# Kernel tuning notes

Measured on AMD Instinct MI355X. Metric: run time of the kernel, lower is better.

## Reference

```python
import jax, jax.numpy as jnp
import numpy as np

N, C, H, L = 10000, 256, 8, 3
D = C // H  # per-head dim
E = 320000


def setup_inputs() -> dict:
    key = jax.random.key(0)
    ks = jax.random.split(key, 12)
    x = jax.random.normal(ks[0], (N, C), dtype=jnp.float32)
    edge_index = jax.random.randint(ks[1], (2, E), 0, N, dtype=jnp.int64)
    s = 0.02
    Wq = jax.random.normal(ks[2], (L, C, C), dtype=jnp.float32) * s
    Wk = jax.random.normal(ks[3], (L, C, C), dtype=jnp.float32) * s
    Wv = jax.random.normal(ks[4], (L, C, C), dtype=jnp.float32) * s
    Ws = jax.random.normal(ks[5], (L, C, C), dtype=jnp.float32) * s
    bq = jax.random.normal(ks[6], (L, C), dtype=jnp.float32) * s
    bk = jax.random.normal(ks[7], (L, C), dtype=jnp.float32) * s
    bv = jax.random.normal(ks[8], (L, C), dtype=jnp.float32) * s
    bs = jax.random.normal(ks[9], (L, C), dtype=jnp.float32) * s
    return {"x": x, "Wq": Wq, "bq": bq, "Wk": Wk, "bk": bk,
            "Wv": Wv, "bv": bv, "Ws": Ws, "bs": bs, "edge_index": edge_index}


def _transformer_conv(x, Wq, bq, Wk, bk, Wv, bv, Ws, bs, src, dst):
    # projections: [N, C] -> [N, H, D]
    q = (x @ Wq + bq).reshape(N, H, D)
    k = (x @ Wk + bk).reshape(N, H, D)
    v = (x @ Wv + bv).reshape(N, H, D)
    # per-edge attention scores: query at target, key/value at source
    score = jnp.einsum('ehd,ehd->eh', q[dst], k[src]) / jnp.sqrt(jnp.float32(D))  # [E, H]
    # scatter softmax over incoming edges per target node
    m = jax.ops.segment_max(score, dst, num_segments=N)            # [N, H]
    a = jnp.exp(score - m[dst])                                    # [E, H]
    denom = jax.ops.segment_sum(a, dst, num_segments=N)           # [N, H]
    alpha = a / (denom[dst] + 1e-16)                               # [E, H]
    # weighted aggregation of values
    msg = alpha[:, :, None] * v[src]                               # [E, H, D]
    out = jax.ops.segment_sum(msg, dst, num_segments=N).reshape(N, C)
    # root/skip connection
    return out + x @ Ws + bs


def reference(x, Wq, bq, Wk, bk, Wv, bv, Ws, bs, edge_index):
    src, dst = edge_index[0], edge_index[1]
    for l in range(L):
        x = _transformer_conv(x, Wq[l], bq[l], Wk[l], bk[l],
                              Wv[l], bv[l], Ws[l], bs[l], src, dst)
    return x
```

## Files before the change

kernel.cpp:

```cpp
#include <hip/hip_runtime.h>
#include <hip/hip_bf16.h>

#define N_NODES 10000
#define C_DIM   256
#define H_HEADS 8
#define D_HEAD  32
#define E_EDGES 320000
#define L_LAYERS 3
#define GN      1024

typedef __attribute__((ext_vector_type(8))) short bf16x8;
typedef __attribute__((ext_vector_type(4))) float f32x4;

__device__ __forceinline__ unsigned short f2b(float f) {
  __hip_bfloat16 h = __float2bfloat16(f);
  return *(unsigned short*)&h;
}

__device__ __forceinline__ float kv_lo(unsigned int w) {
  union { unsigned int u; float f; } c; c.u = w << 16; return c.f;
}
__device__ __forceinline__ float kv_hi(unsigned int w) {
  union { unsigned int u; float f; } c; c.u = w & 0xffff0000u; return c.f;
}

__device__ __forceinline__ float red8(float p) {
  p += __shfl_xor(p, 1);
  p += __shfl_xor(p, 2);
  p += __shfl_xor(p, 4);
  return p;
}

__device__ __forceinline__ float dot4(float4 q, uint4 w) {
  return fmaf(q.x, kv_lo(w.x),
         fmaf(q.y, kv_lo(w.y),
         fmaf(q.z, kv_lo(w.z), q.w * kv_lo(w.w))));
}

__device__ __forceinline__ void gload16(const void* g, void* l) {
  __builtin_amdgcn_global_load_lds(
      (const __attribute__((address_space(1))) unsigned int*)g,
      (__attribute__((address_space(3))) unsigned int*)l, 16, 0, 0);
}

__device__ __forceinline__ int colmap(int mat, int c) {
  if (mat == 0) return c;
  if (mat == 3) return 768 + c;
  return 256 + ((c >> 6) << 7) + ((mat - 1) << 6) + (c & 63);
}

__global__ void hist_kernel(const int* __restrict__ dst, int* __restrict__ deg) {
  int e = blockIdx.x * blockDim.x + threadIdx.x;
  if (e < E_EDGES) atomicAdd(&deg[dst[e]], 1);
}

__global__ __launch_bounds__(1024) void scan_kernel(const int* __restrict__ deg,
                                                    int* __restrict__ row_ptr) {
  __shared__ int part[1024];
  int t = threadIdx.x;
  const int CHUNK = (N_NODES + 1023) / 1024;
  int base = t * CHUNK;
  int s = 0;
  for (int i = 0; i < CHUNK; ++i) {
    int idx = base + i;
    if (idx < N_NODES) s += deg[idx];
  }
  part[t] = s;
  __syncthreads();
  for (int off = 1; off < 1024; off <<= 1) {
    int v = (t >= off) ? part[t - off] : 0;
    __syncthreads();
    part[t] += v;
    __syncthreads();
  }
  int run = (t == 0) ? 0 : part[t - 1];
  for (int i = 0; i < CHUNK; ++i) {
    int idx = base + i;
    if (idx <= N_NODES) {
      row_ptr[idx] = run;
      if (idx < N_NODES) run += deg[idx];
    }
  }
}

__global__ void scatter_kernel(const int* __restrict__ src, const int* __restrict__ dst,
                               const int* __restrict__ row_ptr, int* __restrict__ fill,
                               int* __restrict__ srcs) {
  int e = blockIdx.x * blockDim.x + threadIdx.x;
  if (e < E_EDGES) {
    int d = dst[e];
    int pos = atomicAdd(&fill[d], 1);
    srcs[row_ptr[d] + pos] = src[e];
  }
}

__global__ __launch_bounds__(256) void conv_all_kernel(
    const float* __restrict__ x, __hip_bfloat16* __restrict__ xb,
    const float* __restrict__ Wq, const float* __restrict__ Wk,
    const float* __restrict__ Wv, const float* __restrict__ Ws,
    __hip_bfloat16* __restrict__ Wt,
    const float* __restrict__ bq, const float* __restrict__ bk,
    const float* __restrict__ bv, const float* __restrict__ bs,
    float* __restrict__ biasf) {
  __shared__ float tt[32][33];
  int b = blockIdx.x, t = threadIdx.x;
  if (b < 2500) {
    int i = b * 256 + t;
    float4 f = *(const float4*)&x[(size_t)i * 4];
    union { unsigned short u[4]; uint2 w; } o;
    o.u[0] = f2b(f.x); o.u[1] = f2b(f.y); o.u[2] = f2b(f.z); o.u[3] = f2b(f.w);
    *(uint2*)&xb[(size_t)i * 4] = o.w;
  } else if (b < 3268) {
    int zz = b - 2500;
    int z = zz >> 6, tile = zz & 63;
    int l = z >> 2, mat = z & 3;
    const float* W = (mat == 0 ? Wq : mat == 1 ? Wk : mat == 2 ? Wv : Ws)
                     + (size_t)l * C_DIM * C_DIM;
    int k0 = (tile >> 3) * 32, c0 = (tile & 7) * 32;
    int tx = t & 31, ty = t >> 5;
    for (int i = 0; i < 32; i += 8)
      tt[ty + i][tx] = W[(k0 + ty + i) * C_DIM + c0 + tx];
    __syncthreads();
    for (int i = 0; i < 32; i += 8) {
      int ncol = colmap(mat, c0 + ty + i);
      Wt[(size_t)l * GN * C_DIM + (size_t)ncol * C_DIM + k0 + tx] =
          __float2bfloat16(tt[tx][ty + i]);
    }
  } else {
    int i = (b - 3268) * 256 + t;
    if (i < L_LAYERS * GN) {
      int l = i >> 10, n = i & 1023;
      int mat = n >> 8, c = n & 255;
      const float* bb = (mat == 0 ? bq : mat == 1 ? bk : mat == 2 ? bv : bs);
      biasf[l * GN + colmap(mat, c)] = bb[l * C_DIM + c];
    }
  }
}

__global__ __launch_bounds__(256) void gemm_kernel(
    const __hip_bfloat16* __restrict__ xb,
    const __hip_bfloat16* __restrict__ Wt,
    const float* __restrict__ biasf,
    float* __restrict__ q2,
    unsigned short* __restrict__ kvu,
    float* __restrict__ skip) {
  __shared__ __align__(16) unsigned short SH[16384];
  __hip_bfloat16* As = (__hip_bfloat16*)SH;
  __hip_bfloat16* Bs = (__hip_bfloat16*)(SH + 8192);
  int tid = threadIdx.x;
  int wid = tid >> 6, lane = tid & 63;
  int row0 = blockIdx.x * 128;
  int col0 = blockIdx.y * 128;
  int wr = wid >> 1, wc = wid & 1;
  int lr = lane & 15, lq = lane >> 4;
  int swz = (lr & 7) * 8;

  f32x4 acc[4][4] = {};

  for (int k0 = 0; k0 < C_DIM; k0 += 64) {
#pragma unroll
    for (int j = 0; j < 4; ++j) {
      int c = j * 256 + wid * 64 + lane;
      int arow = c >> 3;
      int kc = 8 * ((c & 7) ^ ((c >> 3) & 7));
      int grow = row0 + arow;
      if (grow > N_NODES - 1) grow = N_NODES - 1;
      gload16(xb + (size_t)grow * C_DIM + k0 + kc, As + (size_t)(j * 256 + wid * 64) * 8);
    }
#pragma unroll
    for (int j = 0; j < 4; ++j) {
      int c = j * 256 + wid * 64 + lane;
      int brow = c >> 3;
      int kc = 8 * ((c & 7) ^ ((c >> 3) & 7));
      gload16(Wt + (size_t)(col0 + brow) * C_DIM + k0 + kc,
              Bs + (size_t)(j * 256 + wid * 64) * 8);
    }
    __syncthreads();

#pragma unroll
    for (int ks = 0; ks < 2; ++ks) {
      bf16x8 fa[4], fb[4];
#pragma unroll
      for (int m = 0; m < 4; ++m)
        fa[m] = *(const bf16x8*)&As[(wr * 64 + m * 16 + lr) * 64 + ((ks * 32 + lq * 8) ^ swz)];
#pragma unroll
      for (int n = 0; n < 4; ++n)
        fb[n] = *(const bf16x8*)&Bs[(wc * 64 + n * 16 + lr) * 64 + ((ks * 32 + lq * 8) ^ swz)];
#pragma unroll
      for (int m = 0; m < 4; ++m)
#pragma unroll
        for (int n = 0; n < 4; ++n)
          acc[m][n] = __builtin_amdgcn_mfma_f32_16x16x32_bf16(fa[m], fb[n], acc[m][n], 0, 0, 0);
    }
    __syncthreads();
  }

  float bias_n[4];
#pragma unroll
  for (int n = 0; n < 4; ++n) bias_n[n] = biasf[col0 + wc * 64 + n * 16 + lr];

  if (col0 >= 256 && col0 < 768) {
    int half = wc;
#pragma unroll
    for (int m = 0; m < 4; ++m) {
#pragma unroll
      for (int n = 0; n < 4; ++n) {
        int chs = n * 16 + lr;
#pragma unroll
        for (int r = 0; r < 4; ++r) {
          int row = wr * 64 + m * 16 + lq * 4 + r;
          SH[row * 128 + chs * 2 + half] = f2b(acc[m][n][r] + bias_n[n]);
        }
      }
    }
    __syncthreads();
    int bl = (col0 - 256) >> 7;
    int sl = bl >> 1;
    int h64 = (bl & 1) * 64;
    unsigned int* kvd = (unsigned int*)kvu;
    int t16 = tid & 15, rbase = tid >> 4;
#pragma unroll
    for (int it = 0; it < 8; ++it) {
      int row = it * 16 + rbase;
      int grow = row0 + row;
      if (grow < N_NODES) {
        uint4 vv = *(const uint4*)&SH[row * 128 + t16 * 8];
        *(uint4*)&kvd[((size_t)sl * N_NODES + grow) * 128 + h64 + t16 * 4] = vv;
      }
    }
  } else {
#pragma unroll
    for (int m = 0; m < 4; ++m) {
#pragma unroll
      for (int n = 0; n < 4; ++n) {
        int colG = col0 + wc * 64 + n * 16 + lr;
#pragma unroll
        for (int r = 0; r < 4; ++r) {
          int grow = row0 + wr * 64 + m * 16 + lq * 4 + r;
          if (grow < N_NODES) {
            float val = acc[m][n][r] + bias_n[n];
            if (col0 < 256) {
              q2[((size_t)(colG >> 7) * N_NODES + grow) * 128 + (colG & 127)] = val;
            } else {
              skip[(size_t)grow * C_DIM + (colG - 768)] = val;
            }
          }
        }
      }
    }
  }
}

__global__ __launch_bounds__(256) void agg_kernel(
    const float* __restrict__ q2,
    const unsigned int* __restrict__ kv2,
    const int* __restrict__ row_ptr, const int* __restrict__ srcs,
    float* __restrict__ out, __hip_bfloat16* __restrict__ xb_next) {
  int b = blockIdx.x;
  int slice = b & 1;
  int wid = threadIdx.x >> 6, lane = threadIdx.x & 63;
  int n = (b >> 1) * 4 + wid;
  int slot = lane >> 5;
  int l4 = (lane & 31) * 4;
  const size_t SB = (size_t)slice * N_NODES * 128;
  const float scl = 0.25503526f;

  float4 qv = *(const float4*)&q2[SB + (size_t)n * 128 + l4];
  qv.x *= scl; qv.y *= scl; qv.z *= scl; qv.w *= scl;
  const unsigned int* kvs = kv2 + SB;

  int beg = row_ptr[n], end = row_ptr[n + 1];
  float l = 0.f;
  float4 a = make_float4(0.f, 0.f, 0.f, 0.f);

  int i = beg;
  int sa1 = 0, sb1 = 0;
  uint4 wa = make_uint4(0, 0, 0, 0), wb = make_uint4(0, 0, 0, 0);
  if (i + 4 <= end) {
    int sa0 = srcs[i + slot], sb0 = srcs[i + 2 + slot];
    wa = *(const uint4*)&kvs[(size_t)sa0 * 128 + l4];
    wb = *(const uint4*)&kvs[(size_t)sb0 * 128 + l4];
    if (i + 8 <= end) { sa1 = srcs[i + 4 + slot]; sb1 = srcs[i + 6 + slot]; }
  }
  while (i + 4 <= end) {
    uint4 na = make_uint4(0, 0, 0, 0), nb = make_uint4(0, 0, 0, 0);
    if (i + 8 <= end) {
      na = *(const uint4*)&kvs[(size_t)sa1 * 128 + l4];
      nb = *(const uint4*)&kvs[(size_t)sb1 * 128 + l4];
      if (i + 12 <= end) {
        sa1 = srcs[i + 8 + slot]; sb1 = srcs[i + 10 + slot];
      }
    }
    float pa = red8(dot4(qv, wa));
    float pb = red8(dot4(qv, wb));
    float ea = exp2f(pa), eb = exp2f(pb);
    l += ea + eb;
    a.x = fmaf(ea, kv_hi(wa.x), fmaf(eb, kv_hi(wb.x), a.x));
    a.y = fmaf(ea, kv_hi(wa.y), fmaf(eb, kv_hi(wb.y), a.y));
    a.z = fmaf(ea, kv_hi(wa.z), fmaf(eb, kv_hi(wb.z), a.z));
    a.w = fmaf(ea, kv_hi(wa.w), fmaf(eb, kv_hi(wb.w), a.w));
    wa = na; wb = nb;
    i += 4;
  }
  for (; i < end; i += 2) {
    int j = i + slot;
    bool valid = j < end;
    int s = srcs[valid ? j : beg];
    uint4 w = *(const uint4*)&kvs[(size_t)s * 128 + l4];
    float p = red8(dot4(qv, w));
    float e = valid ? exp2f(p) : 0.f;
    l += e;
    a.x = fmaf(e, kv_hi(w.x), a.x);
    a.y = fmaf(e, kv_hi(w.y), a.y);
    a.z = fmaf(e, kv_hi(w.z), a.z);
    a.w = fmaf(e, kv_hi(w.w), a.w);
  }

  l   += __shfl_xor(l, 32);
  a.x += __shfl_xor(a.x, 32);
  a.y += __shfl_xor(a.y, 32);
  a.z += __shfl_xor(a.z, 32);
  a.w += __shfl_xor(a.w, 32);

  if (lane < 32) {
    float inv = 1.f / (l + 1e-16f);
    size_t idx = (size_t)n * C_DIM + slice * 128 + l4;
    float4 o = *(const float4*)&out[idx];
    o.x += a.x * inv; o.y += a.y * inv; o.z += a.z * inv; o.w += a.w * inv;
    *(float4*)&out[idx] = o;
    union { unsigned short us[4]; uint2 w; } ob;
    ob.us[0] = f2b(o.x); ob.us[1] = f2b(o.y); ob.us[2] = f2b(o.z); ob.us[3] = f2b(o.w);
    *(uint2*)&xb_next[idx] = ob.w;
  }
}

extern "C" void kernel_launch(void* const* d_in, const int* in_sizes, int n_in,
                              void* d_out, int out_size, void* d_ws, size_t ws_size,
                              hipStream_t stream) {
  const float* x0 = (const float*)d_in[0];
  const float* Wq = (const float*)d_in[1];
  const float* bq = (const float*)d_in[2];
  const float* Wk = (const float*)d_in[3];
  const float* bk = (const float*)d_in[4];
  const float* Wv = (const float*)d_in[5];
  const float* bv = (const float*)d_in[6];
  const float* Ws = (const float*)d_in[7];
  const float* bs = (const float*)d_in[8];
  const int* ei  = (const int*)d_in[9];
  const int* src = ei;
  const int* dst = ei + E_EDGES;
  float* out = (float*)d_out;

  const size_t NC = (size_t)N_NODES * C_DIM;
  __hip_bfloat16* xb = (__hip_bfloat16*)d_ws;
  unsigned int* kvbuf = (unsigned int*)(xb + NC);
  __hip_bfloat16* Wt = (__hip_bfloat16*)(kvbuf + NC);
  float* qbuf  = (float*)(Wt + (size_t)L_LAYERS * GN * C_DIM);
  float* skipA = qbuf + NC;
  float* biasf = skipA + NC;
  int* row_ptr = (int*)(biasf + L_LAYERS * GN);
  int* deg  = row_ptr + (N_NODES + 1);
  int* fill = deg + N_NODES;
  int* srcs = fill + N_NODES;

  (void)hipMemsetAsync(deg, 0, 2 * N_NODES * sizeof(int), stream);
  hist_kernel<<<(E_EDGES + 255) / 256, 256, 0, stream>>>(dst, deg);
  scan_kernel<<<1, 1024, 0, stream>>>(deg, row_ptr);
  scatter_kernel<<<(E_EDGES + 255) / 256, 256, 0, stream>>>(src, dst, row_ptr, fill, srcs);

  conv_all_kernel<<<3281, 256, 0, stream>>>(x0, xb, Wq, Wk, Wv, Ws, Wt,
                                            bq, bk, bv, bs, biasf);

  for (int l = 0; l < L_LAYERS; ++l) {
    float* skip = (l == L_LAYERS - 1) ? out : skipA;
    gemm_kernel<<<dim3((N_NODES + 127) / 128, GN / 128), 256, 0, stream>>>(
        xb, Wt + (size_t)l * GN * C_DIM, biasf + l * GN, qbuf,
        (unsigned short*)kvbuf, skip);
    agg_kernel<<<dim3(2 * (N_NODES / 4)), 256, 0, stream>>>(
        qbuf, kvbuf, row_ptr, srcs, skip, xb);
  }
}
```

Measured before the change: 201.5 us.

## Split fused attention aggregation into separate score and aggregation kernels with K/V split

Splits the interleaved K/V bf16 buffer into separate K and V arrays, and replaces the single fused score+softmax+aggregate kernel with two passes. The first computes exp scores per edge and head, storing them and per-node denominators. The second gathers V rows weighted by the stored scores. Each gather now reads contiguous 16-byte rows of only K or only V, with 16 lanes per edge and 4 edges in flight. The cost is an extra kernel launch, a round-trip of per-edge scores through global memory, and re-reading the CSR indices.

```diff
diff --git a/kernel.cpp b/kernel.cpp
--- a/kernel.cpp
+++ b/kernel.cpp
@@ -22,19 +22,6 @@
 }
 __device__ __forceinline__ float kv_hi(unsigned int w) {
   union { unsigned int u; float f; } c; c.u = w & 0xffff0000u; return c.f;
-}
-
-__device__ __forceinline__ float red8(float p) {
-  p += __shfl_xor(p, 1);
-  p += __shfl_xor(p, 2);
-  p += __shfl_xor(p, 4);
-  return p;
-}
-
-__device__ __forceinline__ float dot4(float4 q, uint4 w) {
-  return fmaf(q.x, kv_lo(w.x),
-         fmaf(q.y, kv_lo(w.y),
-         fmaf(q.z, kv_lo(w.z), q.w * kv_lo(w.w))));
 }
 
 __device__ __forceinline__ void gload16(const void* g, void* l) {
@@ -142,7 +129,8 @@
     const __hip_bfloat16* __restrict__ Wt,
     const float* __restrict__ biasf,
     float* __restrict__ q2,
-    unsigned short* __restrict__ kvu,
+    unsigned short* __restrict__ k2,
+    unsigned short* __restrict__ v2,
     float* __restrict__ skip) {
   __shared__ __align__(16) unsigned short SH[16384];
   __hip_bfloat16* As = (__hip_bfloat16*)SH;
@@ -209,7 +197,7 @@
 #pragma unroll
         for (int r = 0; r < 4; ++r) {
           int row = wr * 64 + m * 16 + lq * 4 + r;
-          SH[row * 128 + chs * 2 + half] = f2b(acc[m][n][r] + bias_n[n]);
+          SH[row * 128 + half * 64 + chs] = f2b(acc[m][n][r] + bias_n[n]);
         }
       }
     }
@@ -217,7 +205,6 @@
     int bl = (col0 - 256) >> 7;
     int sl = bl >> 1;
     int h64 = (bl & 1) * 64;
-    unsigned int* kvd = (unsigned int*)kvu;
     int t16 = tid & 15, rbase = tid >> 4;
 #pragma unroll
     for (int it = 0; it < 8; ++it) {
@@ -225,7 +212,10 @@
       int grow = row0 + row;
       if (grow < N_NODES) {
         uint4 vv = *(const uint4*)&SH[row * 128 + t16 * 8];
-        *(uint4*)&kvd[((size_t)sl * N_NODES + grow) * 128 + h64 + t16 * 4] = vv;
+        size_t base = ((size_t)sl * N_NODES + grow) * 128 + h64;
+        unsigned short* dp = (t16 < 8) ? (k2 + base + t16 * 8)
+                                       : (v2 + base + (t16 - 8) * 8);
+        *(uint4*)dp = vv;
       }
     }
   } else {
@@ -251,86 +241,140 @@
   }
 }
 
-__global__ __launch_bounds__(256) void agg_kernel(
+__global__ __launch_bounds__(256) void score_kernel(
     const float* __restrict__ q2,
-    const unsigned int* __restrict__ kv2,
+    const unsigned short* __restrict__ k2,
+    const int* __restrict__ row_ptr, const int* __restrict__ srcs,
+    float* __restrict__ esc,
+    float* __restrict__ dnm) {
+  int b = blockIdx.x;
+  int slice = b & 1;
+  int wid = threadIdx.x >> 6, lane = threadIdx.x & 63;
+  int n = (b >> 1) * 4 + wid;
+  int slot = lane >> 4;
+  int le = lane & 15;
+  int h = le >> 2;
+  const float scl = 0.25503526f;
+  const unsigned short* ks = k2 + (size_t)slice * N_NODES * 128;
+  float* escS = esc + (size_t)slice * E_EDGES * 4;
+
+  const float* qrow = &q2[((size_t)slice * N_NODES + n) * 128 + le * 8];
+  float4 qa = *(const float4*)qrow;
+  float4 qb = *(const float4*)(qrow + 4);
+  qa.x *= scl; qa.y *= scl; qa.z *= scl; qa.w *= scl;
+  qb.x *= scl; qb.y *= scl; qb.z *= scl; qb.w *= scl;
+
+  int beg = row_ptr[n], end = row_ptr[n + 1];
+  float l = 0.f;
+
+  if (beg < end) {
+    int j0 = beg + slot;
+    int sc = srcs[j0 < end ? j0 : beg];
+    uint4 w = *(const uint4*)&ks[(size_t)sc * 128 + le * 8];
+    int j1 = beg + 4 + slot;
+    int sn = srcs[j1 < end ? j1 : beg];
+    for (int i = beg; i < end; i += 4) {
+      uint4 wn = w;
+      bool more = (i + 4) < end;
+      if (more) {
+        wn = *(const uint4*)&ks[(size_t)sn * 128 + le * 8];
+        int j2 = i + 8 + slot;
+        sn = srcs[j2 < end ? j2 : beg];
+      }
+      float p = fmaf(qa.x, kv_lo(w.x), fmaf(qa.y, kv_hi(w.x),
+                fmaf(qa.z, kv_lo(w.y), fmaf(qa.w, kv_hi(w.y),
+                fmaf(qb.x, kv_lo(w.z), fmaf(qb.y, kv_hi(w.z),
+                fmaf(qb.z, kv_lo(w.w), qb.w * kv_hi(w.w))))))));
+      p += __shfl_xor(p, 1);
+      p += __shfl_xor(p, 2);
+      bool valid = (i + slot) < end;
+      float e = valid ? exp2f(p) : 0.f;
+      l += e;
+      if (valid && (lane & 3) == 0)
+        escS[(size_t)(i + slot) * 4 + h] = e;
+      w = wn;
+    }
+  }
+  l += __shfl_xor(l, 16);
+  l += __shfl_xor(l, 32);
+  if (lane < 16 && (lane & 3) == 0)
+    dnm[((size_t)slice * N_NODES + n) * 4 + h] = l;
+}
+
+__global__ __launch_bounds__(256) void aggr_kernel(
+    const unsigned short* __restrict__ v2,
+    const float* __restrict__ esc,
+    const float* __restrict__ dnm,
     const int* __restrict__ row_ptr, const int* __restrict__ srcs,
     float* __restrict__ out, __hip_bfloat16* __restrict__ xb_next) {
   int b = blockIdx.x;
   int slice = b & 1;
   int wid = threadIdx.x >> 6, lane = threadIdx.x & 63;
   int n = (b >> 1) * 4 + wid;
-  int slot = lane >> 5;
-  int l4 = (lane & 31) * 4;
-  const size_t SB = (size_t)slice * N_NODES * 128;
-  const float scl = 0.25503526f;
-
-  float4 qv = *(const float4*)&q2[SB + (size_t)n * 128 + l4];
-  qv.x *= scl; qv.y *= scl; qv.z *= scl; qv.w *= scl;
-  const unsigned int* kvs = kv2 + SB;
+  int slot = lane >> 4;
+  int le = lane & 15;
+  int h = le >> 2;
+  const unsigned short* vs = v2 + (size_t)slice * N_NODES * 128;
+  const float* escS = esc + (size_t)slice * E_EDGES * 4;
+
+  float inv = 1.f / (dnm[((size_t)slice * N_NODES + n) * 4 + h] + 1e-16f);
 
   int beg = row_ptr[n], end = row_ptr[n + 1];
-  float l = 0.f;
-  float4 a = make_float4(0.f, 0.f, 0.f, 0.f);
-
-  int i = beg;
-  int sa1 = 0, sb1 = 0;
-  uint4 wa = make_uint4(0, 0, 0, 0), wb = make_uint4(0, 0, 0, 0);
-  if (i + 4 <= end) {
-    int sa0 = srcs[i + slot], sb0 = srcs[i + 2 + slot];
-    wa = *(const uint4*)&kvs[(size_t)sa0 * 128 + l4];
-    wb = *(const uint4*)&kvs[(size_t)sb0 * 128 + l4];
-    if (i + 8 <= end) { sa1 = srcs[i + 4 + slot]; sb1 = srcs[i + 6 + slot]; }
-  }
-  while (i + 4 <= end) {
-    uint4 na = make_uint4(0, 0, 0, 0), nb = make_uint4(0, 0, 0, 0);
-    if (i + 8 <= end) {
-      na = *(const uint4*)&kvs[(size_t)sa1 * 128 + l4];
-      nb = *(const uint4*)&kvs[(size_t)sb1 * 128 + l4];
-      if (i + 12 <= end) {
-        sa1 = srcs[i + 8 + slot]; sb1 = srcs[i + 10 + slot];
+  float a0 = 0.f, a1 = 0.f, a2 = 0.f, a3 = 0.f;
+  float a4 = 0.f, a5 = 0.f, a6 = 0.f, a7 = 0.f;
+
+  if (beg < end) {
+    int j0 = beg + slot;
+    int jc = j0 < end ? j0 : beg;
+    int sc = srcs[jc];
+    uint4 w = *(const uint4*)&vs[(size_t)sc * 128 + le * 8];
+    float ec = escS[(size_t)jc * 4 + h];
+    int j1 = beg + 4 + slot;
+    int jn = j1 < end ? j1 : beg;
+    int sn = srcs[jn];
+    for (int i = beg; i < end; i += 4) {
+      uint4 wn = w; float en = 0.f;
+      bool more = (i + 4) < end;
+      if (more) {
+        wn = *(const uint4*)&vs[(size_t)sn * 128 + le * 8];
+        en = escS[(size_t)jn * 4 + h];
+        int j2 = i + 8 + slot;
+        jn = j2 < end ? j2 : beg;
+        sn = srcs[jn];
       }
-    }
-    float pa = red8(dot4(qv, wa));
-    float pb = red8(dot4(qv, wb));
-    float ea = exp2f(pa), eb = exp2f(pb);
-    l += ea + eb;
-    a.x = fmaf(ea, kv_hi(wa.x), fmaf(eb, kv_hi(wb.x), a.x));
-    a.y = fmaf(ea, kv_hi(wa.y), fmaf(eb, kv_hi(wb.y), a.y));
-    a.z = fmaf(ea, kv_hi(wa.z), fmaf(eb, kv_hi(wb.z), a.z));
-    a.w = fmaf(ea, kv_hi(wa.w), fmaf(eb, kv_hi(wb.w), a.w));
-    wa = na; wb = nb;
-    i += 4;
-  }
-  for (; i < end; i += 2) {
-    int j = i + slot;
-    bool valid = j < end;
-    int s = srcs[valid ? j : beg];
-    uint4 w = *(const uint4*)&kvs[(size_t)s * 128 + l4];
-    float p = red8(dot4(qv, w));
-    float e = valid ? exp2f(p) : 0.f;
-    l += e;
-    a.x = fmaf(e, kv_hi(w.x), a.x);
-    a.y = fmaf(e, kv_hi(w.y), a.y);
-    a.z = fmaf(e, kv_hi(w.z), a.z);
-    a.w = fmaf(e, kv_hi(w.w), a.w);
-  }
-
-  l   += __shfl_xor(l, 32);
-  a.x += __shfl_xor(a.x, 32);
-  a.y += __shfl_xor(a.y, 32);
-  a.z += __shfl_xor(a.z, 32);
-  a.w += __shfl_xor(a.w, 32);
-
-  if (lane < 32) {
-    float inv = 1.f / (l + 1e-16f);
-    size_t idx = (size_t)n * C_DIM + slice * 128 + l4;
-    float4 o = *(const float4*)&out[idx];
-    o.x += a.x * inv; o.y += a.y * inv; o.z += a.z * inv; o.w += a.w * inv;
-    *(float4*)&out[idx] = o;
-    union { unsigned short us[4]; uint2 w; } ob;
-    ob.us[0] = f2b(o.x); ob.us[1] = f2b(o.y); ob.us[2] = f2b(o.z); ob.us[3] = f2b(o.w);
-    *(uint2*)&xb_next[idx] = ob.w;
+      float e = ((i + slot) < end) ? ec : 0.f;
+      a0 = fmaf(e, kv_lo(w.x), a0);
+      a1 = fmaf(e, kv_hi(w.x), a1);
+      a2 = fmaf(e, kv_lo(w.y), a2);
+      a3 = fmaf(e, kv_hi(w.y), a3);
+      a4 = fmaf(e, kv_lo(w.z), a4);
+      a5 = fmaf(e, kv_hi(w.z), a5);
+      a6 = fmaf(e, kv_lo(w.w), a6);
+      a7 = fmaf(e, kv_hi(w.w), a7);
+      w = wn; ec = en;
+    }
+  }
+  a0 += __shfl_xor(a0, 16); a0 += __shfl_xor(a0, 32);
+  a1 += __shfl_xor(a1, 16); a1 += __shfl_xor(a1, 32);
+  a2 += __shfl_xor(a2, 16); a2 += __shfl_xor(a2, 32);
+  a3 += __shfl_xor(a3, 16); a3 += __shfl_xor(a3, 32);
+  a4 += __shfl_xor(a4, 16); a4 += __shfl_xor(a4, 32);
+  a5 += __shfl_xor(a5, 16); a5 += __shfl_xor(a5, 32);
+  a6 += __shfl_xor(a6, 16); a6 += __shfl_xor(a6, 32);
+  a7 += __shfl_xor(a7, 16); a7 += __shfl_xor(a7, 32);
+
+  if (lane < 16) {
+    size_t idx = (size_t)n * C_DIM + slice * 128 + le * 8;
+    float4 o1 = *(const float4*)&out[idx];
+    float4 o2 = *(const float4*)&out[idx + 4];
+    o1.x += a0 * inv; o1.y += a1 * inv; o1.z += a2 * inv; o1.w += a3 * inv;
+    o2.x += a4 * inv; o2.y += a5 * inv; o2.z += a6 * inv; o2.w += a7 * inv;
+    *(float4*)&out[idx] = o1;
+    *(float4*)&out[idx + 4] = o2;
+    union { unsigned short us[8]; uint4 w; } ob;
+    ob.us[0] = f2b(o1.x); ob.us[1] = f2b(o1.y); ob.us[2] = f2b(o1.z); ob.us[3] = f2b(o1.w);
+    ob.us[4] = f2b(o2.x); ob.us[5] = f2b(o2.y); ob.us[6] = f2b(o2.z); ob.us[7] = f2b(o2.w);
+    *(uint4*)&xb_next[idx] = ob.w;
   }
 }
 
@@ -353,12 +397,15 @@
 
   const size_t NC = (size_t)N_NODES * C_DIM;
   __hip_bfloat16* xb = (__hip_bfloat16*)d_ws;
-  unsigned int* kvbuf = (unsigned int*)(xb + NC);
-  __hip_bfloat16* Wt = (__hip_bfloat16*)(kvbuf + NC);
+  unsigned short* k2 = (unsigned short*)(xb + NC);
+  unsigned short* v2 = k2 + NC;
+  __hip_bfloat16* Wt = (__hip_bfloat16*)(v2 + NC);
   float* qbuf  = (float*)(Wt + (size_t)L_LAYERS * GN * C_DIM);
   float* skipA = qbuf + NC;
   float* biasf = skipA + NC;
-  int* row_ptr = (int*)(biasf + L_LAYERS * GN);
+  float* esc   = biasf + L_LAYERS * GN;
+  float* dnm   = esc + (size_t)2 * E_EDGES * 4;
+  int* row_ptr = (int*)(dnm + (size_t)2 * N_NODES * 4);
   int* deg  = row_ptr + (N_NODES + 1);
   int* fill = deg + N_NODES;
   int* srcs = fill + N_NODES;
@@ -374,9 +421,10 @@
   for (int l = 0; l < L_LAYERS; ++l) {
     float* skip = (l == L_LAYERS - 1) ? out : skipA;
     gemm_kernel<<<dim3((N_NODES + 127) / 128, GN / 128), 256, 0, stream>>>(
-        xb, Wt + (size_t)l * GN * C_DIM, biasf + l * GN, qbuf,
-        (unsigned short*)kvbuf, skip);
-    agg_kernel<<<dim3(2 * (N_NODES / 4)), 256, 0, stream>>>(
-        qbuf, kvbuf, row_ptr, srcs, skip, xb);
-  }
-}
+        xb, Wt + (size_t)l * GN * C_DIM, biasf + l * GN, qbuf, k2, v2, skip);
+    score_kernel<<<dim3(2 * (N_NODES / 4)), 256, 0, stream>>>(
+        qbuf, k2, row_ptr, srcs, esc, dnm);
+    aggr_kernel<<<dim3(2 * (N_NODES / 4)), 256, 0, stream>>>(
+        v2, esc, dnm, row_ptr, srcs, skip, xb);
+  }
+}
```

Measured after the change: 233.2 us. 15.7% more time.

## Process four nodes per wavefront in aggregation and prescale source indices to byte offsets

Applied to the files above, without the earlier changes.

Each wavefront in the aggregation kernel now handles four consecutive destination nodes instead of one. The row pointers, query vectors and the first pair of source indices for all four nodes are loaded up front, and the grid shrinks to a quarter of its former size. Source indices are stored pre-shifted by 9 (times 512 bytes, one kv row) at scatter time, which removes the multiply from the address computation. This cuts per-block launch overhead and overlaps index latency across nodes, at the cost of more registers, less parallelism and possibly more load imbalance.

```diff
diff --git a/kernel.cpp b/kernel.cpp
--- a/kernel.cpp
+++ b/kernel.cpp
@@ -90,7 +90,7 @@
   if (e < E_EDGES) {
     int d = dst[e];
     int pos = atomicAdd(&fill[d], 1);
-    srcs[row_ptr[d] + pos] = src[e];
+    srcs[row_ptr[d] + pos] = src[e] << 9;
   }
 }
 
@@ -259,78 +259,100 @@
   int b = blockIdx.x;
   int slice = b & 1;
   int wid = threadIdx.x >> 6, lane = threadIdx.x & 63;
-  int n = (b >> 1) * 4 + wid;
+  int n0 = (b >> 1) * 16 + wid * 4;
   int slot = lane >> 5;
   int l4 = (lane & 31) * 4;
   const size_t SB = (size_t)slice * N_NODES * 128;
   const float scl = 0.25503526f;
-
-  float4 qv = *(const float4*)&q2[SB + (size_t)n * 128 + l4];
-  qv.x *= scl; qv.y *= scl; qv.z *= scl; qv.w *= scl;
-  const unsigned int* kvs = kv2 + SB;
-
-  int beg = row_ptr[n], end = row_ptr[n + 1];
-  float l = 0.f;
-  float4 a = make_float4(0.f, 0.f, 0.f, 0.f);
-
-  int i = beg;
-  int sa1 = 0, sb1 = 0;
-  uint4 wa = make_uint4(0, 0, 0, 0), wb = make_uint4(0, 0, 0, 0);
-  if (i + 4 <= end) {
-    int sa0 = srcs[i + slot], sb0 = srcs[i + 2 + slot];
-    wa = *(const uint4*)&kvs[(size_t)sa0 * 128 + l4];
-    wb = *(const uint4*)&kvs[(size_t)sb0 * 128 + l4];
-    if (i + 8 <= end) { sa1 = srcs[i + 4 + slot]; sb1 = srcs[i + 6 + slot]; }
-  }
-  while (i + 4 <= end) {
-    uint4 na = make_uint4(0, 0, 0, 0), nb = make_uint4(0, 0, 0, 0);
-    if (i + 8 <= end) {
-      na = *(const uint4*)&kvs[(size_t)sa1 * 128 + l4];
-      nb = *(const uint4*)&kvs[(size_t)sb1 * 128 + l4];
-      if (i + 12 <= end) {
-        sa1 = srcs[i + 8 + slot]; sb1 = srcs[i + 10 + slot];
+  const char* kvb = (const char*)(kv2 + SB) + l4 * 4;
+
+  int rp[5];
+#pragma unroll
+  for (int m = 0; m < 5; ++m) rp[m] = row_ptr[n0 + m];
+
+  float4 qv[4];
+#pragma unroll
+  for (int m = 0; m < 4; ++m) {
+    qv[m] = *(const float4*)&q2[SB + (size_t)(n0 + m) * 128 + l4];
+    qv[m].x *= scl; qv[m].y *= scl; qv[m].z *= scl; qv[m].w *= scl;
+  }
+
+  int f0[4], f1[4];
+#pragma unroll
+  for (int m = 0; m < 4; ++m) {
+    int beg = rp[m], end = rp[m + 1];
+    int ja = beg + slot;     if (ja >= end) ja = beg;
+    int jb = beg + 2 + slot; if (jb >= end) jb = beg;
+    if (ja >= E_EDGES) ja = 0;
+    if (jb >= E_EDGES) jb = 0;
+    f0[m] = srcs[ja];
+    f1[m] = srcs[jb];
+  }
+
+#pragma unroll
+  for (int m = 0; m < 4; ++m) {
+    int beg = rp[m], end = rp[m + 1];
+    float l = 0.f;
+    float4 a = make_float4(0.f, 0.f, 0.f, 0.f);
+
+    int i = beg;
+    int sa1 = 0, sb1 = 0;
+    uint4 wa = make_uint4(0, 0, 0, 0), wb = make_uint4(0, 0, 0, 0);
+    if (i + 4 <= end) {
+      wa = *(const uint4*)(kvb + f0[m]);
+      wb = *(const uint4*)(kvb + f1[m]);
+      if (i + 8 <= end) { sa1 = srcs[i + 4 + slot]; sb1 = srcs[i + 6 + slot]; }
+    }
+    while (i + 4 <= end) {
+      uint4 na = make_uint4(0, 0, 0, 0), nb = make_uint4(0, 0, 0, 0);
+      if (i + 8 <= end) {
+        na = *(const uint4*)(kvb + sa1);
+        nb = *(const uint4*)(kvb + sb1);
+        if (i + 12 <= end) {
+          sa1 = srcs[i + 8 + slot]; sb1 = srcs[i + 10 + slot];
+        }
       }
-    }
-    float pa = red8(dot4(qv, wa));
-    float pb = red8(dot4(qv, wb));
-    float ea = exp2f(pa), eb = exp2f(pb);
-    l += ea + eb;
-    a.x = fmaf(ea, kv_hi(wa.x), fmaf(eb, kv_hi(wb.x), a.x));
-    a.y = fmaf(ea, kv_hi(wa.y), fmaf(eb, kv_hi(wb.y), a.y));
-    a.z = fmaf(ea, kv_hi(wa.z), fmaf(eb, kv_hi(wb.z), a.z));
-    a.w = fmaf(ea, kv_hi(wa.w), fmaf(eb, kv_hi(wb.w), a.w));
-    wa = na; wb = nb;
-    i += 4;
-  }
-  for (; i < end; i += 2) {
-    int j = i + slot;
-    bool valid = j < end;
-    int s = srcs[valid ? j : beg];
-    uint4 w = *(const uint4*)&kvs[(size_t)s * 128 + l4];
-    float p = red8(dot4(qv, w));
-    float e = valid ? exp2f(p) : 0.f;
-    l += e;
-    a.x = fmaf(e, kv_hi(w.x), a.x);
-    a.y = fmaf(e, kv_hi(w.y), a.y);
-    a.z = fmaf(e, kv_hi(w.z), a.z);
-    a.w = fmaf(e, kv_hi(w.w), a.w);
-  }
-
-  l   += __shfl_xor(l, 32);
-  a.x += __shfl_xor(a.x, 32);
-  a.y += __shfl_xor(a.y, 32);
-  a.z += __shfl_xor(a.z, 32);
-  a.w += __shfl_xor(a.w, 32);
-
-  if (lane < 32) {
-    float inv = 1.f / (l + 1e-16f);
-    size_t idx = (size_t)n * C_DIM + slice * 128 + l4;
-    float4 o = *(const float4*)&out[idx];
-    o.x += a.x * inv; o.y += a.y * inv; o.z += a.z * inv; o.w += a.w * inv;
-    *(float4*)&out[idx] = o;
-    union { unsigned short us[4]; uint2 w; } ob;
-    ob.us[0] = f2b(o.x); ob.us[1] = f2b(o.y); ob.us[2] = f2b(o.z); ob.us[3] = f2b(o.w);
-    *(uint2*)&xb_next[idx] = ob.w;
+      float pa = red8(dot4(qv[m], wa));
+      float pb = red8(dot4(qv[m], wb));
+      float ea = exp2f(pa), eb = exp2f(pb);
+      l += ea + eb;
+      a.x = fmaf(ea, kv_hi(wa.x), fmaf(eb, kv_hi(wb.x), a.x));
+      a.y = fmaf(ea, kv_hi(wa.y), fmaf(eb, kv_hi(wb.y), a.y));
+      a.z = fmaf(ea, kv_hi(wa.z), fmaf(eb, kv_hi(wb.z), a.z));
+      a.w = fmaf(ea, kv_hi(wa.w), fmaf(eb, kv_hi(wb.w), a.w));
+      wa = na; wb = nb;
+      i += 4;
+    }
+    for (; i < end; i += 2) {
+      int j = i + slot;
+      bool valid = j < end;
+      int s = srcs[valid ? j : beg];
+      uint4 w = *(const uint4*)(kvb + s);
+      float p = red8(dot4(qv[m], w));
+      float e = valid ? exp2f(p) : 0.f;
+      l += e;
+      a.x = fmaf(e, kv_hi(w.x), a.x);
+      a.y = fmaf(e, kv_hi(w.y), a.y);
+      a.z = fmaf(e, kv_hi(w.z), a.z);
+      a.w = fmaf(e, kv_hi(w.w), a.w);
+    }
+
+    l   += __shfl_xor(l, 32);
+    a.x += __shfl_xor(a.x, 32);
+    a.y += __shfl_xor(a.y, 32);
+    a.z += __shfl_xor(a.z, 32);
+    a.w += __shfl_xor(a.w, 32);
+
+    if (lane < 32) {
+      float inv = 1.f / (l + 1e-16f);
+      size_t idx = (size_t)(n0 + m) * C_DIM + slice * 128 + l4;
+      float4 o = *(const float4*)&out[idx];
+      o.x += a.x * inv; o.y += a.y * inv; o.z += a.z * inv; o.w += a.w * inv;
+      *(float4*)&out[idx] = o;
+      union { unsigned short us[4]; uint2 w; } ob;
+      ob.us[0] = f2b(o.x); ob.us[1] = f2b(o.y); ob.us[2] = f2b(o.z); ob.us[3] = f2b(o.w);
+      *(uint2*)&xb_next[idx] = ob.w;
+    }
   }
 }
 
@@ -376,7 +398,7 @@
     gemm_kernel<<<dim3((N_NODES + 127) / 128, GN / 128), 256, 0, stream>>>(
         xb, Wt + (size_t)l * GN * C_DIM, biasf + l * GN, qbuf,
         (unsigned short*)kvbuf, skip);
-    agg_kernel<<<dim3(2 * (N_NODES / 4)), 256, 0, stream>>>(
+    agg_kernel<<<dim3(2 * (N_NODES / 16)), 256, 0, stream>>>(
         qbuf, kvbuf, row_ptr, srcs, skip, xb);
   }
 }
```

New measurement: 223.5 us. +10.9%, slower.
